# Kernel optimization log

Hardware: AMD Instinct MI355X
Metric: run time of the kernel (lower is better)

The kernel has to match this reference:

```python
import jax, jax.numpy as jnp
import numpy as np

ROPE_BASE = 10000.0

def _rope_cos_sin(T, dh, dtype):
    inv_freq = 1.0 / (ROPE_BASE ** (jnp.arange(0, dh, 2, dtype=jnp.float32) / dh))
    t = jnp.arange(T, dtype=jnp.float32)
    freqs = jnp.outer(t, inv_freq)                      # [T, dh/2]
    emb = jnp.concatenate([freqs, freqs], axis=-1)      # [T, dh]
    return jnp.cos(emb).astype(dtype), jnp.sin(emb).astype(dtype)

def _rotate_half(x):
    x1, x2 = jnp.split(x, 2, axis=-1)
    return jnp.concatenate([-x2, x1], axis=-1)

def setup_inputs() -> dict:
    key = jax.random.key(0)
    k1, k2, k3 = jax.random.split(key, 3)
    B, T, D = 2, 2048, 2048
    x = jax.random.normal(k1, (B, T, D), dtype=jnp.float32)
    w_qkv = jax.random.normal(k2, (3 * D, D), dtype=jnp.float32) * (D ** -0.5)
    w_proj = jax.random.normal(k3, (D, D), dtype=jnp.float32) * (D ** -0.5)
    return {"x": x, "w_qkv": w_qkv, "w_proj": w_proj}

def reference(x, w_qkv, w_proj):
    B, T, D = x.shape
    H = 16
    Dh = D // H
    scale = Dh ** -0.5
    qkv = x @ w_qkv.T                                   # [B,T,3D]
    qkv = qkv.reshape(B, T, 3, H, Dh).transpose(2, 0, 3, 1, 4)  # [3,B,H,T,Dh]
    q, k, v = qkv[0], qkv[1], qkv[2]
    cos, sin = _rope_cos_sin(T, Dh, x.dtype)            # [T,Dh] each, offset=0
    q = q * cos + _rotate_half(q) * sin
    k = k * cos + _rotate_half(k) * sin
    attn = jnp.einsum('bhqd,bhkd->bhqk', q, k) * scale  # [B,H,T,T]
    causal = jnp.triu(jnp.full((T, T), -jnp.inf, dtype=attn.dtype), k=1)
    attn = jax.nn.softmax(attn + causal, axis=-1)
    out = jnp.einsum('bhqk,bhkd->bhqd', attn, v)        # [B,H,T,Dh]
    out = out.transpose(0, 2, 1, 3).reshape(B, T, D)
    return out @ w_proj.T
```

## Files before the change

### kernel.cpp

```cpp
#include <hip/hip_runtime.h>
#include <stdint.h>

typedef unsigned short u16;
typedef unsigned int   u32;
typedef __attribute__((ext_vector_type(8))) __bf16 bf16x8;
typedef __attribute__((ext_vector_type(4))) float  f32x4;

#define MFMA_16x16x32_BF16(a, b, c) __builtin_amdgcn_mfma_f32_16x16x32_bf16((a), (b), (c), 0, 0, 0)

__device__ __forceinline__ u16 f2b(float f) {
    u32 u = __builtin_bit_cast(u32, f);
    u32 r = (u + 0x7FFFu + ((u >> 16) & 1u)) >> 16;
    return (u16)r;
}
__device__ __forceinline__ float b2f(u16 h) {
    u32 u = ((u32)h) << 16;
    return __builtin_bit_cast(float, u);
}

__device__ __forceinline__ void gload_lds16(const void* g, void* l) {
    __builtin_amdgcn_global_load_lds(
        (const __attribute__((address_space(1))) u32*)g,
        (__attribute__((address_space(3))) u32*)l,
        16, 0, 0);
}

__global__ __launch_bounds__(256) void cast3(const float* __restrict__ x,
                                             const float* __restrict__ wq,
                                             const float* __restrict__ wp,
                                             u16* __restrict__ xb,
                                             u16* __restrict__ wqb,
                                             u16* __restrict__ wpb) {
    const int n1 = 8388608, n2 = 12582912, n3 = 4194304;
    const int total4 = (n1 + n2 + n3) / 4;
    for (int i = blockIdx.x * blockDim.x + threadIdx.x; i < total4;
         i += gridDim.x * blockDim.x) {
        int e = i * 4;
        const float* src; u16* dst; int off;
        if (e < n1)            { src = x;  dst = xb;  off = e; }
        else if (e < n1 + n2)  { src = wq; dst = wqb; off = e - n1; }
        else                   { src = wp; dst = wpb; off = e - n1 - n2; }
        float4 v = *(const float4*)(src + off);
        ushort4 o;
        o.x = f2b(v.x); o.y = f2b(v.y); o.z = f2b(v.z); o.w = f2b(v.w);
        *(ushort4*)(dst + off) = o;
    }
}

template <int OUT_BF16>
__global__ __launch_bounds__(256) void gemm_bt(const u16* __restrict__ A,
                                               const u16* __restrict__ Bt,
                                               void* __restrict__ Cout,
                                               int M, int N, int K) {
    __shared__ u16 Al[128 * 64];
    __shared__ u16 Bl[128 * 64];
    const int tid  = threadIdx.x;
    const int w    = tid >> 6;
    const int lane = tid & 63;
    const int quad = lane >> 4;
    const int l16  = lane & 15;
    const int m0 = blockIdx.y * 128;
    const int n0 = blockIdx.x * 128;
    const int wm = (w >> 1) * 64;
    const int wn = (w & 1) * 64;

    f32x4 acc[4][4];
#pragma unroll
    for (int i = 0; i < 4; i++) {
#pragma unroll
        for (int j = 0; j < 4; j++) acc[i][j] = (f32x4){0.f, 0.f, 0.f, 0.f};
    }

    const u16* Abase = A + (size_t)(m0 + (tid >> 3)) * K + (tid & 7) * 8;
    const u16* Bbase = Bt + (size_t)(n0 + (tid >> 3)) * K + (tid & 7) * 8;
    char* AlB = (char*)Al + w * 1024;
    char* BlB = (char*)Bl + w * 1024;

    for (int k0 = 0; k0 < K; k0 += 64) {
        __syncthreads();
#pragma unroll
        for (int i = 0; i < 4; i++) {
            gload_lds16(Abase + (size_t)i * 32 * K + k0, AlB + i * 4096);
            gload_lds16(Bbase + (size_t)i * 32 * K + k0, BlB + i * 4096);
        }
        __syncthreads();
#pragma unroll
        for (int ks = 0; ks < 2; ks++) {
            bf16x8 Af[4];
#pragma unroll
            for (int mi = 0; mi < 4; mi++)
                Af[mi] = *(const bf16x8*)&Al[(wm + mi * 16 + l16) * 64 + ks * 32 + quad * 8];
#pragma unroll
            for (int ni = 0; ni < 4; ni++) {
                bf16x8 Bf = *(const bf16x8*)&Bl[(wn + ni * 16 + l16) * 64 + ks * 32 + quad * 8];
#pragma unroll
                for (int mi = 0; mi < 4; mi++)
                    acc[mi][ni] = MFMA_16x16x32_BF16(Af[mi], Bf, acc[mi][ni]);
            }
        }
    }

    const int row0 = m0 + wm + quad * 4;
    const int col0 = n0 + wn + l16;
#pragma unroll
    for (int mi = 0; mi < 4; mi++) {
#pragma unroll
        for (int r = 0; r < 4; r++) {
            size_t rowb = (size_t)(row0 + mi * 16 + r) * N;
#pragma unroll
            for (int ni = 0; ni < 4; ni++) {
                float v = acc[mi][ni][r];
                if (OUT_BF16) ((u16*)Cout)[rowb + col0 + ni * 16] = f2b(v);
                else          ((float*)Cout)[rowb + col0 + ni * 16] = v;
            }
        }
    }
}

__global__ __launch_bounds__(256) void rope_qk(const u16* __restrict__ qkv,
                                               u16* __restrict__ Q,
                                               u16* __restrict__ K) {
    const int bt = blockIdx.x;
    const int b = bt >> 11, t = bt & 2047;
    const u16* row = qkv + (size_t)bt * 6144;
    const int tid = threadIdx.x;

#pragma unroll
    for (int it = 0; it < 8; it++) {
        int p   = it * 256 + tid;
        int qk  = p >> 10;
        int rem = p & 1023;
        int h   = rem >> 6;
        int i   = rem & 63;
        float x1 = b2f(row[qk * 2048 + h * 128 + i]);
        float x2 = b2f(row[qk * 2048 + h * 128 + i + 64]);
        float inv = expf(-0.14391156f * (float)i);
        float th  = (float)t * inv;
        float s, c;
        sincosf(th, &s, &c);
        float o1 = x1 * c - x2 * s;
        float o2 = x2 * c + x1 * s;
        u16* dst = (qk ? K : Q) + ((size_t)((b * 16 + h) * 2048 + t)) * 128;
        dst[i]      = f2b(o1);
        dst[i + 64] = f2b(o2);
    }
}

__global__ __launch_bounds__(256) void vtrans(const u16* __restrict__ qkv,
                                              u16* __restrict__ VT) {
    __shared__ u16 S[64 * 136];
    const int tc = blockIdx.x;
    const int bh = blockIdx.y;
    const int b = bh >> 4, h = bh & 15;
    const int tid = threadIdx.x;

#pragma unroll
    for (int i = 0; i < 4; i++) {
        int idx = i * 256 + tid;
        int t  = idx >> 4;
        int d8 = (idx & 15) * 8;
        uint4 v = *(const uint4*)(qkv + ((size_t)(b * 2048 + tc * 64 + t)) * 6144
                                      + 4096 + h * 128 + d8);
        *(uint4*)&S[t * 136 + d8] = v;
    }
    __syncthreads();
#pragma unroll
    for (int i = 0; i < 4; i++) {
        int idx = i * 256 + tid;
        int d  = idx >> 3;
        int t8 = (idx & 7) * 8;
        u16 tmp[8];
#pragma unroll
        for (int j = 0; j < 8; j++) tmp[j] = S[(t8 + j) * 136 + d];
        *(uint4*)(VT + ((size_t)(bh * 128 + d)) * 2048 + tc * 64 + t8) = *(uint4*)tmp;
    }
}

__global__ __launch_bounds__(256) void attn(const u16* __restrict__ Q,
                                            const u16* __restrict__ Kg,
                                            const u16* __restrict__ VTg,
                                            u16* __restrict__ O) {
    __shared__ u16 Kl[64 * 128];
    __shared__ u16 Vt[128 * 64];
    __shared__ u16 Pl[4 * 16 * 68];

    const int tid  = threadIdx.x;
    const int w    = tid >> 6;
    const int lane = tid & 63;
    const int quad = lane >> 4;
    const int l16  = lane & 15;
    const int pair = blockIdx.x;
    const int bh   = blockIdx.y;
    const int b = bh >> 4, h = bh & 15;
    const size_t base = (size_t)bh * 2048 * 128;
    const u16* Qb  = Q + base;
    const u16* Kb  = Kg + base;
    const u16* VTb = VTg + base;
    u16* Plw = Pl + w * 16 * 68;
    const float scale = 0.08838834764831845f;

    for (int s = 0; s < 2; s++) {
        const int qt   = s ? (31 - pair) : pair;
        const int q0   = qt * 64;
        const int row0 = q0 + w * 16;

        bf16x8 Qf[4];
#pragma unroll
        for (int kk = 0; kk < 4; kk++)
            Qf[kk] = *(const bf16x8*)&Qb[(size_t)(row0 + l16) * 128 + kk * 32 + quad * 8];

        f32x4 Oacc[8];
#pragma unroll
        for (int ni = 0; ni < 8; ni++) Oacc[ni] = (f32x4){0.f, 0.f, 0.f, 0.f};
        float mrow[4], lrow[4];
#pragma unroll
        for (int r = 0; r < 4; r++) { mrow[r] = -INFINITY; lrow[r] = 0.f; }

        const int nkt = qt + 1;
        for (int kt = 0; kt < nkt; kt++) {
            const int kt0 = kt * 64;
            __syncthreads();
            {
                const u16* ksrc = Kb + (size_t)(kt0 + (tid >> 4)) * 128 + (tid & 15) * 8;
                char* kdst = (char*)Kl + w * 1024;
#pragma unroll
                for (int i = 0; i < 4; i++)
                    gload_lds16(ksrc + (size_t)i * 16 * 128, kdst + i * 4096);
            }
            {
                const u16* vsrc = VTb + (size_t)(w * 8 + (lane >> 3)) * 2048 + kt0 + (lane & 7) * 8;
                char* vdst = (char*)Vt + w * 1024;
#pragma unroll
                for (int i = 0; i < 4; i++)
                    gload_lds16(vsrc + (size_t)i * 32 * 2048, vdst + i * 4096);
            }
            __syncthreads();

            f32x4 S4[4];
#pragma unroll
            for (int ni = 0; ni < 4; ni++) {
                S4[ni] = (f32x4){0.f, 0.f, 0.f, 0.f};
#pragma unroll
                for (int kk = 0; kk < 4; kk++) {
                    bf16x8 Kf = *(const bf16x8*)&Kl[(ni * 16 + l16) * 128 + kk * 32 + quad * 8];
                    S4[ni] = MFMA_16x16x32_BF16(Qf[kk], Kf, S4[ni]);
                }
            }

            const bool needs_mask = (kt0 + 63) > row0;
            float tmax[4] = {-1e30f, -1e30f, -1e30f, -1e30f};
#pragma unroll
            for (int ni = 0; ni < 4; ni++) {
                int kg = kt0 + ni * 16 + l16;
#pragma unroll
                for (int r = 0; r < 4; r++) {
                    float sv = S4[ni][r] * scale;
                    if (needs_mask) {
                        int qg = row0 + quad * 4 + r;
                        sv = (kg > qg) ? -1e30f : sv;
                    }
                    S4[ni][r] = sv;
                    tmax[r] = fmaxf(tmax[r], sv);
                }
            }
#pragma unroll
            for (int r = 0; r < 4; r++) {
#pragma unroll
                for (int off = 1; off < 16; off <<= 1)
                    tmax[r] = fmaxf(tmax[r], __shfl_xor(tmax[r], off));
            }
            float alpha[4];
#pragma unroll
            for (int r = 0; r < 4; r++) {
                float mnew = fmaxf(mrow[r], tmax[r]);
                alpha[r] = __expf(mrow[r] - mnew);
                mrow[r] = mnew;
            }
            float tsum[4] = {0.f, 0.f, 0.f, 0.f};
#pragma unroll
            for (int ni = 0; ni < 4; ni++) {
#pragma unroll
                for (int r = 0; r < 4; r++) {
                    float p = __expf(S4[ni][r] - mrow[r]);
                    S4[ni][r] = p;
                    tsum[r] += p;
                }
            }
#pragma unroll
            for (int r = 0; r < 4; r++) {
#pragma unroll
                for (int off = 1; off < 16; off <<= 1)
                    tsum[r] += __shfl_xor(tsum[r], off);
                lrow[r] = lrow[r] * alpha[r] + tsum[r];
            }
#pragma unroll
            for (int ni = 0; ni < 8; ni++) {
#pragma unroll
                for (int r = 0; r < 4; r++) Oacc[ni][r] *= alpha[r];
            }
#pragma unroll
            for (int ni = 0; ni < 4; ni++) {
#pragma unroll
                for (int r = 0; r < 4; r++)
                    Plw[(quad * 4 + r) * 68 + ni * 16 + l16] = f2b(S4[ni][r]);
            }

            bf16x8 Pf[2];
#pragma unroll
            for (int kk = 0; kk < 2; kk++)
                Pf[kk] = *(const bf16x8*)&Plw[l16 * 68 + kk * 32 + quad * 8];
#pragma unroll
            for (int ni = 0; ni < 8; ni++) {
#pragma unroll
                for (int kk = 0; kk < 2; kk++) {
                    bf16x8 Vf = *(const bf16x8*)&Vt[(ni * 16 + l16) * 64 + kk * 32 + quad * 8];
                    Oacc[ni] = MFMA_16x16x32_BF16(Pf[kk], Vf, Oacc[ni]);
                }
            }
        }

#pragma unroll
        for (int r = 0; r < 4; r++) {
            int t = row0 + quad * 4 + r;
            float inv = 1.0f / lrow[r];
            size_t rowb = ((size_t)(b * 2048 + t)) * 2048 + (size_t)(h * 128);
#pragma unroll
            for (int ni = 0; ni < 8; ni++)
                O[rowb + ni * 16 + l16] = f2b(Oacc[ni][r] * inv);
        }
    }
}

extern "C" void kernel_launch(void* const* d_in, const int* in_sizes, int n_in,
                              void* d_out, int out_size, void* d_ws, size_t ws_size,
                              hipStream_t stream) {
    const float* x  = (const float*)d_in[0];
    const float* wq = (const float*)d_in[1];
    const float* wp = (const float*)d_in[2];

    char* ws = (char*)d_ws;
    u16* xb   = (u16*)(ws + 0);
    u16* wqb  = (u16*)(ws + 16777216);
    u16* wpb  = (u16*)(ws + 41943040);
    u16* qkvb = (u16*)(ws + 50331648);
    u16* Qr   = (u16*)(ws + 100663296);
    u16* Kr   = (u16*)(ws + 117440512);
    u16* VTt  = (u16*)(ws + 134217728);
    u16* Ob   = (u16*)(ws + 50331648);
    if (ws_size < 150994944) return;

    cast3<<<2048, 256, 0, stream>>>(x, wq, wp, xb, wqb, wpb);
    gemm_bt<1><<<dim3(48, 32), 256, 0, stream>>>(xb, wqb, qkvb, 4096, 6144, 2048);
    rope_qk<<<4096, 256, 0, stream>>>(qkvb, Qr, Kr);
    vtrans<<<dim3(32, 32), 256, 0, stream>>>(qkvb, VTt);
    attn<<<dim3(16, 32), 256, 0, stream>>>(Qr, Kr, VTt, Ob);
    gemm_bt<0><<<dim3(16, 32), 256, 0, stream>>>(Ob, wpb, (float*)d_out, 4096, 2048, 2048);
}
```

Baseline: 474.7 us.

## Double-buffer K/V tiles and compute transposed scores for per-lane row softmax

The attention kernel now keeps two LDS buffers for K and V^T and prefetches the next key tile while the current one is being computed. This replaces the old pattern of loading then immediately waiting at a barrier each iteration. The QK^T MFMA is also swapped to compute S^T, so each lane owns one query row. That cuts the row max to two cross-quad shuffles, lets the row sum be reduced once at the end, and allows packed ushort4 stores of P into a repadded LDS buffer. The cost is double the K/V LDS footprint, which may reduce occupancy, plus a few extra shuffles to broadcast alpha and 1/l back to the accumulator layout.

```diff
diff --git a/kernel.cpp b/kernel.cpp
--- a/kernel.cpp
+++ b/kernel.cpp
@@ -180,9 +180,9 @@
                                             const u16* __restrict__ Kg,
                                             const u16* __restrict__ VTg,
                                             u16* __restrict__ O) {
-    __shared__ u16 Kl[64 * 128];
-    __shared__ u16 Vt[128 * 64];
-    __shared__ u16 Pl[4 * 16 * 68];
+    __shared__ u16 Kl[2][64 * 128];
+    __shared__ u16 Vt[2][128 * 64];
+    __shared__ u16 Pl[4 * 16 * 76];
 
     const int tid  = threadIdx.x;
     const int w    = tid >> 6;
@@ -196,8 +196,11 @@
     const u16* Qb  = Q + base;
     const u16* Kb  = Kg + base;
     const u16* VTb = VTg + base;
-    u16* Plw = Pl + w * 16 * 68;
+    u16* Plw = Pl + w * 16 * 76;
     const float scale = 0.08838834764831845f;
+
+    const int krow = tid >> 4, kcol = (tid & 15) * 8;
+    const int vrow = w * 8 + (lane >> 3), vcol = (lane & 7) * 8;
 
     for (int s = 0; s < 2; s++) {
         const int qt   = s ? (31 - pair) : pair;
@@ -212,121 +215,136 @@
         f32x4 Oacc[8];
 #pragma unroll
         for (int ni = 0; ni < 8; ni++) Oacc[ni] = (f32x4){0.f, 0.f, 0.f, 0.f};
-        float mrow[4], lrow[4];
-#pragma unroll
-        for (int r = 0; r < 4; r++) { mrow[r] = -INFINITY; lrow[r] = 0.f; }
+        float mrow = -1e30f, lrow = 0.f;
 
         const int nkt = qt + 1;
+
+        __syncthreads();
+        {
+            const u16* ksrc = Kb + (size_t)krow * 128 + kcol;
+            char* kdst = (char*)Kl[0] + w * 1024;
+            const u16* vsrc = VTb + (size_t)vrow * 2048 + vcol;
+            char* vdst = (char*)Vt[0] + w * 1024;
+#pragma unroll
+            for (int i = 0; i < 4; i++) {
+                gload_lds16(ksrc + (size_t)i * 16 * 128, kdst + i * 4096);
+                gload_lds16(vsrc + (size_t)i * 32 * 2048, vdst + i * 4096);
+            }
+        }
+
         for (int kt = 0; kt < nkt; kt++) {
             const int kt0 = kt * 64;
+            const int cur = kt & 1;
             __syncthreads();
-            {
-                const u16* ksrc = Kb + (size_t)(kt0 + (tid >> 4)) * 128 + (tid & 15) * 8;
-                char* kdst = (char*)Kl + w * 1024;
-#pragma unroll
-                for (int i = 0; i < 4; i++)
+
+            if (kt + 1 < nkt) {
+                const int kt1 = kt0 + 64;
+                const u16* ksrc = Kb + (size_t)(kt1 + krow) * 128 + kcol;
+                char* kdst = (char*)Kl[cur ^ 1] + w * 1024;
+                const u16* vsrc = VTb + (size_t)vrow * 2048 + kt1 + vcol;
+                char* vdst = (char*)Vt[cur ^ 1] + w * 1024;
+#pragma unroll
+                for (int i = 0; i < 4; i++) {
                     gload_lds16(ksrc + (size_t)i * 16 * 128, kdst + i * 4096);
-            }
-            {
-                const u16* vsrc = VTb + (size_t)(w * 8 + (lane >> 3)) * 2048 + kt0 + (lane & 7) * 8;
-                char* vdst = (char*)Vt + w * 1024;
-#pragma unroll
-                for (int i = 0; i < 4; i++)
                     gload_lds16(vsrc + (size_t)i * 32 * 2048, vdst + i * 4096);
-            }
-            __syncthreads();
-
-            f32x4 S4[4];
-#pragma unroll
-            for (int ni = 0; ni < 4; ni++) {
-                S4[ni] = (f32x4){0.f, 0.f, 0.f, 0.f};
-#pragma unroll
-                for (int kk = 0; kk < 4; kk++) {
-                    bf16x8 Kf = *(const bf16x8*)&Kl[(ni * 16 + l16) * 128 + kk * 32 + quad * 8];
-                    S4[ni] = MFMA_16x16x32_BF16(Qf[kk], Kf, S4[ni]);
+                }
+            }
+
+            const u16* Klc = Kl[cur];
+            const u16* Vtc = Vt[cur];
+
+            f32x4 ST[4];
+#pragma unroll
+            for (int mi = 0; mi < 4; mi++) ST[mi] = (f32x4){0.f, 0.f, 0.f, 0.f};
+#pragma unroll
+            for (int kk = 0; kk < 4; kk++) {
+#pragma unroll
+                for (int mi = 0; mi < 4; mi++) {
+                    bf16x8 Kf = *(const bf16x8*)&Klc[(mi * 16 + l16) * 128 + kk * 32 + quad * 8];
+                    ST[mi] = MFMA_16x16x32_BF16(Kf, Qf[kk], ST[mi]);
                 }
             }
 
             const bool needs_mask = (kt0 + 63) > row0;
-            float tmax[4] = {-1e30f, -1e30f, -1e30f, -1e30f};
-#pragma unroll
-            for (int ni = 0; ni < 4; ni++) {
-                int kg = kt0 + ni * 16 + l16;
+            const int qg = row0 + l16;
+            float tmax = -1e30f;
+#pragma unroll
+            for (int mi = 0; mi < 4; mi++) {
 #pragma unroll
                 for (int r = 0; r < 4; r++) {
-                    float sv = S4[ni][r] * scale;
+                    float sv = ST[mi][r] * scale;
                     if (needs_mask) {
-                        int qg = row0 + quad * 4 + r;
+                        int kg = kt0 + mi * 16 + quad * 4 + r;
                         sv = (kg > qg) ? -1e30f : sv;
                     }
-                    S4[ni][r] = sv;
-                    tmax[r] = fmaxf(tmax[r], sv);
-                }
-            }
-#pragma unroll
-            for (int r = 0; r < 4; r++) {
-#pragma unroll
-                for (int off = 1; off < 16; off <<= 1)
-                    tmax[r] = fmaxf(tmax[r], __shfl_xor(tmax[r], off));
-            }
-            float alpha[4];
-#pragma unroll
-            for (int r = 0; r < 4; r++) {
-                float mnew = fmaxf(mrow[r], tmax[r]);
-                alpha[r] = __expf(mrow[r] - mnew);
-                mrow[r] = mnew;
-            }
-            float tsum[4] = {0.f, 0.f, 0.f, 0.f};
-#pragma unroll
-            for (int ni = 0; ni < 4; ni++) {
+                    ST[mi][r] = sv;
+                    tmax = fmaxf(tmax, sv);
+                }
+            }
+            tmax = fmaxf(tmax, __shfl_xor(tmax, 16));
+            tmax = fmaxf(tmax, __shfl_xor(tmax, 32));
+
+            float mnew  = fmaxf(mrow, tmax);
+            float alpha = __expf(mrow - mnew);
+            mrow = mnew;
+
+            float tsum = 0.f;
+#pragma unroll
+            for (int mi = 0; mi < 4; mi++) {
 #pragma unroll
                 for (int r = 0; r < 4; r++) {
-                    float p = __expf(S4[ni][r] - mrow[r]);
-                    S4[ni][r] = p;
-                    tsum[r] += p;
-                }
-            }
-#pragma unroll
-            for (int r = 0; r < 4; r++) {
-#pragma unroll
-                for (int off = 1; off < 16; off <<= 1)
-                    tsum[r] += __shfl_xor(tsum[r], off);
-                lrow[r] = lrow[r] * alpha[r] + tsum[r];
-            }
+                    float p = __expf(ST[mi][r] - mnew);
+                    ST[mi][r] = p;
+                    tsum += p;
+                }
+            }
+            lrow = lrow * alpha + tsum;
+
+#pragma unroll
+            for (int mi = 0; mi < 4; mi++) {
+                ushort4 pk;
+                pk.x = f2b(ST[mi][0]); pk.y = f2b(ST[mi][1]);
+                pk.z = f2b(ST[mi][2]); pk.w = f2b(ST[mi][3]);
+                *(ushort4*)&Plw[l16 * 76 + mi * 16 + quad * 4] = pk;
+            }
+
+            float aRow[4];
+#pragma unroll
+            for (int r = 0; r < 4; r++) aRow[r] = __shfl(alpha, quad * 4 + r);
 #pragma unroll
             for (int ni = 0; ni < 8; ni++) {
 #pragma unroll
-                for (int r = 0; r < 4; r++) Oacc[ni][r] *= alpha[r];
-            }
-#pragma unroll
-            for (int ni = 0; ni < 4; ni++) {
-#pragma unroll
-                for (int r = 0; r < 4; r++)
-                    Plw[(quad * 4 + r) * 68 + ni * 16 + l16] = f2b(S4[ni][r]);
+                for (int r = 0; r < 4; r++) Oacc[ni][r] *= aRow[r];
             }
 
             bf16x8 Pf[2];
 #pragma unroll
             for (int kk = 0; kk < 2; kk++)
-                Pf[kk] = *(const bf16x8*)&Plw[l16 * 68 + kk * 32 + quad * 8];
-#pragma unroll
-            for (int ni = 0; ni < 8; ni++) {
-#pragma unroll
-                for (int kk = 0; kk < 2; kk++) {
-                    bf16x8 Vf = *(const bf16x8*)&Vt[(ni * 16 + l16) * 64 + kk * 32 + quad * 8];
+                Pf[kk] = *(const bf16x8*)&Plw[l16 * 76 + kk * 32 + quad * 8];
+#pragma unroll
+            for (int kk = 0; kk < 2; kk++) {
+#pragma unroll
+                for (int ni = 0; ni < 8; ni++) {
+                    bf16x8 Vf = *(const bf16x8*)&Vtc[(ni * 16 + l16) * 64 + kk * 32 + quad * 8];
                     Oacc[ni] = MFMA_16x16x32_BF16(Pf[kk], Vf, Oacc[ni]);
                 }
             }
         }
+
+        lrow += __shfl_xor(lrow, 16);
+        lrow += __shfl_xor(lrow, 32);
+        float inv = 1.0f / lrow;
+        float iRow[4];
+#pragma unroll
+        for (int r = 0; r < 4; r++) iRow[r] = __shfl(inv, quad * 4 + r);
 
 #pragma unroll
         for (int r = 0; r < 4; r++) {
             int t = row0 + quad * 4 + r;
-            float inv = 1.0f / lrow[r];
             size_t rowb = ((size_t)(b * 2048 + t)) * 2048 + (size_t)(h * 128);
 #pragma unroll
             for (int ni = 0; ni < 8; ni++)
-                O[rowb + ni * 16 + l16] = f2b(Oacc[ni][r] * inv);
+                O[rowb + ni * 16 + l16] = f2b(Oacc[ni][r] * iRow[r]);
         }
     }
 }
```

After: 458.9 us. 3.3% less time.
